# Kernel tuning notes

Measured on AMD Instinct MI355X. Metric: run time of the kernel, lower is better.

## Reference

```python
import jax, jax.numpy as jnp
import numpy as np

D_MODEL = 1024
N_HEADS = 16
RANK = 128
N_COMPRESS = 16
N_KNOWLEDGE = 32768
KNOWLEDGE_K = 8
B, S = 4, 1024
EPS = 1e-5


def setup_inputs() -> dict:
    key = jax.random.key(0)
    ks = jax.random.split(key, 16)
    inp = {
        'x': jax.random.normal(ks[0], (B, S, D_MODEL), jnp.float32),
        'mask': jnp.tril(jnp.ones((S, S), bool))[None, None],  # causal [1,1,S,S]
        'compress_neurons': jax.random.normal(ks[1], (N_COMPRESS, D_MODEL, RANK), jnp.float32) / np.sqrt(D_MODEL),
        'knowledge_K': jax.random.normal(ks[2], (N_KNOWLEDGE, RANK), jnp.float32) * 0.02,
        'knowledge_V': jax.random.normal(ks[3], (N_KNOWLEDGE, D_MODEL), jnp.float32) * 0.02,
        'router_Q': jax.random.normal(ks[4], (D_MODEL, N_COMPRESS), jnp.float32) * 0.02,
        'router_K': jax.random.normal(ks[5], (D_MODEL, N_COMPRESS), jnp.float32) * 0.02,
        'router_V': jax.random.normal(ks[6], (D_MODEL, N_COMPRESS), jnp.float32) * 0.02,
        'router_M': jax.random.normal(ks[7], (D_MODEL, N_COMPRESS), jnp.float32) * 0.02,
        'W_Q': jax.random.normal(ks[8], (RANK, D_MODEL), jnp.float32) / np.sqrt(RANK),
        'W_K': jax.random.normal(ks[9], (RANK, D_MODEL), jnp.float32) / np.sqrt(RANK),
        'W_V': jax.random.normal(ks[10], (RANK, D_MODEL), jnp.float32) / np.sqrt(RANK),
        'W_O': jax.random.normal(ks[11], (D_MODEL, D_MODEL), jnp.float32) / np.sqrt(D_MODEL),
        'ln1_g': jnp.ones((D_MODEL,), jnp.float32),
        'ln1_b': jnp.zeros((D_MODEL,), jnp.float32),
        'ln2_g': jnp.ones((D_MODEL,), jnp.float32),
        'ln2_b': jnp.zeros((D_MODEL,), jnp.float32),
    }
    return inp


def _layernorm(x, g, b):
    mu = x.mean(-1, keepdims=True)
    var = ((x - mu) ** 2).mean(-1, keepdims=True)
    return (x - mu) * jax.lax.rsqrt(var + EPS) * g + b


def _compress(x, router_W, neurons):
    # x: [B,S,D]; router_W: [D,N]; neurons: [N,D,R]
    weights = jax.nn.softmax(x @ router_W, axis=-1)               # [B,S,N]
    all_proj = jnp.einsum('bsd,ndr->bsnr', x, neurons)            # [B,S,N,R]
    return jnp.einsum('bsnr,bsn->bsr', all_proj, weights)         # [B,S,R]


def reference(x, mask, compress_neurons, knowledge_K, knowledge_V,
              router_Q, router_K, router_V, router_M,
              W_Q, W_K, W_V, W_O, ln1_g, ln1_b, ln2_g, ln2_b):
    d_head = D_MODEL // N_HEADS
    h = _layernorm(x, ln1_g, ln1_b)
    # soft-routed low-rank compression for Q/K/V
    hQ = _compress(h, router_Q, compress_neurons)
    hK = _compress(h, router_K, compress_neurons)
    hV = _compress(h, router_V, compress_neurons)
    Q = (hQ @ W_Q).reshape(B, S, N_HEADS, d_head).transpose(0, 2, 1, 3)
    K = (hK @ W_K).reshape(B, S, N_HEADS, d_head).transpose(0, 2, 1, 3)
    V = (hV @ W_V).reshape(B, S, N_HEADS, d_head).transpose(0, 2, 1, 3)
    scores = jnp.einsum('bhqd,bhkd->bhqk', Q, K) / np.sqrt(d_head)
    scores = jnp.where(mask, scores, -jnp.inf)
    attn = jax.nn.softmax(scores, axis=-1)
    attn_out = jnp.einsum('bhqk,bhkd->bhqd', attn, V)
    attn_out = attn_out.transpose(0, 2, 1, 3).reshape(B, S, D_MODEL)
    x = x + attn_out @ W_O
    # knowledge memory
    h2 = _layernorm(x, ln2_g, ln2_b)
    Qm = _compress(h2, router_M, compress_neurons)                # [B,S,R]
    kscores = Qm @ knowledge_K.T / np.sqrt(RANK)                  # [B,S,NK]
    topk_scores, topk_idx = jax.lax.top_k(kscores, KNOWLEDGE_K)
    kweights = jax.nn.softmax(topk_scores, axis=-1)               # [B,S,k]
    selected_V = knowledge_V[topk_idx]                            # [B,S,k,D]
    mem_out = jnp.einsum('bskd,bsk->bsd', selected_V, kweights)
    return x + mem_out
```

## Files before the change

### kernel.cpp

```cpp
#include <hip/hip_runtime.h>
#include <math.h>

#define DM     1024
#define RANK   128
#define NCMP   16
#define NKNOW  32768
#define TOPK   8
#define NROWS  4096
#define NEG_BIG -3.0e38f
#define TK_SPLIT 32
#define TK_KEYS (NKNOW / TK_SPLIT)

typedef __attribute__((ext_vector_type(8))) short s8v;
typedef __attribute__((ext_vector_type(4))) float f4v;

__device__ __forceinline__ unsigned short f2bf(float f) {
  union { float fl; unsigned u; } v; v.fl = f;
  return (unsigned short)((v.u + 0x7FFFu + ((v.u >> 16) & 1u)) >> 16);
}
__device__ __forceinline__ f4v mfma16(s8v a, s8v b, f4v c) {
  return __builtin_amdgcn_mfma_f32_16x16x32_bf16(a, b, c, 0, 0, 0);
}
__device__ __forceinline__ unsigned umed3(unsigned a, unsigned b, unsigned c) {
  unsigned d;
  asm("v_med3_u32 %0, %1, %2, %3" : "=v"(d) : "v"(a), "v"(b), "v"(c));
  return d;
}

__global__ __launch_bounds__(256) void ln_kernel(const float* __restrict__ x,
                                                 const float* __restrict__ g,
                                                 const float* __restrict__ b,
                                                 float* __restrict__ o,
                                                 unsigned short* __restrict__ obf) {
  __shared__ float red1[4], red2[4];
  const int row = blockIdx.x, t = threadIdx.x;
  const float4 v = reinterpret_cast<const float4*>(x + (size_t)row * DM)[t];
  float s = v.x + v.y + v.z + v.w;
#pragma unroll
  for (int m = 1; m <= 32; m <<= 1) s += __shfl_xor(s, m);
  if ((t & 63) == 0) red1[t >> 6] = s;
  __syncthreads();
  const float mu = (red1[0] + red1[1] + red1[2] + red1[3]) * (1.0f / DM);
  const float dx = v.x - mu, dy = v.y - mu, dz = v.z - mu, dw = v.w - mu;
  float ss = dx * dx + dy * dy + dz * dz + dw * dw;
#pragma unroll
  for (int m = 1; m <= 32; m <<= 1) ss += __shfl_xor(ss, m);
  if ((t & 63) == 0) red2[t >> 6] = ss;
  __syncthreads();
  const float var = (red2[0] + red2[1] + red2[2] + red2[3]) * (1.0f / DM);
  const float inv = rsqrtf(var + 1e-5f);
  const float4 g4 = reinterpret_cast<const float4*>(g)[t];
  const float4 b4 = reinterpret_cast<const float4*>(b)[t];
  float4 r;
  r.x = dx * inv * g4.x + b4.x;
  r.y = dy * inv * g4.y + b4.y;
  r.z = dz * inv * g4.z + b4.z;
  r.w = dw * inv * g4.w + b4.w;
  reinterpret_cast<float4*>(o + (size_t)row * DM)[t] = r;
  ushort4 u = make_ushort4(f2bf(r.x), f2bf(r.y), f2bf(r.z), f2bf(r.w));
  reinterpret_cast<ushort4*>(obf + (size_t)row * DM)[t] = u;
}

__global__ __launch_bounds__(256) void tcvt_kernel(const float* __restrict__ in,
                                                   unsigned short* __restrict__ out,
                                                   int K, int N) {
  __shared__ float ld[32][33];
  const int bb = blockIdx.z;
  const int k0 = blockIdx.y * 32, n0 = blockIdx.x * 32;
  const int t = threadIdx.x;
  const float* ib = in + (size_t)bb * K * N;
  unsigned short* ob = out + (size_t)bb * K * N;
  const int kl = t >> 3, nl = (t & 7) * 4;
  const float4 v = *reinterpret_cast<const float4*>(&ib[(size_t)(k0 + kl) * N + n0 + nl]);
  ld[kl][nl] = v.x; ld[kl][nl + 1] = v.y; ld[kl][nl + 2] = v.z; ld[kl][nl + 3] = v.w;
  __syncthreads();
  const int nw = t >> 3, kw = (t & 7) * 4;
  ushort4 o = make_ushort4(f2bf(ld[kw][nw]), f2bf(ld[kw + 1][nw]),
                           f2bf(ld[kw + 2][nw]), f2bf(ld[kw + 3][nw]));
  *reinterpret_cast<ushort4*>(&ob[(size_t)(n0 + nw) * K + k0 + kw]) = o;
}

__global__ __launch_bounds__(256) void vtr_kernel(const unsigned short* __restrict__ V,
                                                  unsigned short* __restrict__ Vt) {
  __shared__ unsigned short ld[32][40];
  const int bh = blockIdx.z, b = bh >> 4, hh = bh & 15;
  const int s0 = blockIdx.x * 32, d0 = blockIdx.y * 32;
  const int t = threadIdx.x;
  const int r = t >> 3, c = (t & 7) * 4;
  *reinterpret_cast<ushort4*>(&ld[r][c]) =
      *reinterpret_cast<const ushort4*>(&V[(size_t)(b * 1024 + s0 + r) * DM + hh * 64 + d0 + c]);
  __syncthreads();
  ushort4 o;
  o.x = ld[c + 0][r]; o.y = ld[c + 1][r]; o.z = ld[c + 2][r]; o.w = ld[c + 3][r];
  *reinterpret_cast<ushort4*>(&Vt[((size_t)bh * 64 + d0 + r) * 1024 + s0 + c]) = o;
}

__global__ __launch_bounds__(256) void cvt_kernel(const float* __restrict__ in,
                                                  unsigned short* __restrict__ out, int n8) {
  const int i = blockIdx.x * 256 + threadIdx.x;
  if (i < n8) {
    const float4 a = reinterpret_cast<const float4*>(in)[2 * i];
    const float4 b = reinterpret_cast<const float4*>(in)[2 * i + 1];
    reinterpret_cast<ushort4*>(out)[2 * i] =
        make_ushort4(f2bf(a.x), f2bf(a.y), f2bf(a.z), f2bf(a.w));
    reinterpret_cast<ushort4*>(out)[2 * i + 1] =
        make_ushort4(f2bf(b.x), f2bf(b.y), f2bf(b.z), f2bf(b.w));
  }
}

__global__ __launch_bounds__(256) void router3_kernel(const float* __restrict__ h,
                                                      const float* __restrict__ R0,
                                                      const float* __restrict__ R1,
                                                      const float* __restrict__ R2,
                                                      float* __restrict__ w0,
                                                      float* __restrict__ w1,
                                                      float* __restrict__ w2) {
  __shared__ float hs[DM];
  __shared__ float red[3][16][17];
  const int row = blockIdx.x, t = threadIdx.x;
  reinterpret_cast<float4*>(hs)[t] = reinterpret_cast<const float4*>(h + (size_t)row * DM)[t];
  __syncthreads();
  const int o = t & 15, seg = t >> 4;
  float a0 = 0.f, a1 = 0.f, a2 = 0.f;
  for (int d = seg * 64; d < seg * 64 + 64; ++d) {
    const float hv = hs[d];
    a0 += hv * R0[d * NCMP + o];
    a1 += hv * R1[d * NCMP + o];
    a2 += hv * R2[d * NCMP + o];
  }
  red[0][seg][o] = a0; red[1][seg][o] = a1; red[2][seg][o] = a2;
  __syncthreads();
  if (t < 48) {
    const int g = t >> 4, oo = t & 15;
    float dot = 0.f;
#pragma unroll
    for (int s = 0; s < 16; ++s) dot += red[g][s][oo];
    float m = dot;
#pragma unroll
    for (int msk = 1; msk < 16; msk <<= 1) m = fmaxf(m, __shfl_xor(m, msk));
    const float e = __expf(dot - m);
    float ssum = e;
#pragma unroll
    for (int msk = 1; msk < 16; msk <<= 1) ssum += __shfl_xor(ssum, msk);
    float* wp = (g == 0) ? w0 : (g == 1) ? w1 : w2;
    wp[(size_t)row * NCMP + oo] = e / ssum;
  }
}

__global__ __launch_bounds__(256) void router_kernel(const float* __restrict__ h,
                                                     const float* __restrict__ R,
                                                     float* __restrict__ w) {
  __shared__ float hs[DM];
  __shared__ float red[16][17];
  const int row = blockIdx.x, t = threadIdx.x;
  reinterpret_cast<float4*>(hs)[t] = reinterpret_cast<const float4*>(h + (size_t)row * DM)[t];
  __syncthreads();
  const int o = t & 15, seg = t >> 4;
  float acc = 0.f;
  for (int d = seg * 64; d < seg * 64 + 64; ++d) acc += hs[d] * R[d * NCMP + o];
  red[seg][o] = acc;
  __syncthreads();
  if (t < 16) {
    float dot = 0.f;
#pragma unroll
    for (int s = 0; s < 16; ++s) dot += red[s][t];
    float m = dot;
#pragma unroll
    for (int msk = 1; msk < 16; msk <<= 1) m = fmaxf(m, __shfl_xor(m, msk));
    const float e = __expf(dot - m);
    float ssum = e;
#pragma unroll
    for (int msk = 1; msk < 16; msk <<= 1) ssum += __shfl_xor(ssum, msk);
    w[(size_t)row * NCMP + t] = e / ssum;
  }
}

template <bool OUT_BF16, bool RES>
__global__ __launch_bounds__(256) void mfma_nt(const unsigned short* __restrict__ A,
                                               const unsigned short* __restrict__ B,
                                               float* __restrict__ Cf,
                                               unsigned short* __restrict__ Cb,
                                               const float* __restrict__ res,
                                               int M, int N, int K, int bshift) {
  __shared__ unsigned short As[128 * 72];
  __shared__ unsigned short Bs[128 * 72];
  const int t = threadIdx.x;
  const int lane = t & 63, w = t >> 6;
  const int wm = w >> 1, wn = w & 1;
  const int bm = blockIdx.y, bn = blockIdx.x;
  const int l15 = lane & 15, l4 = lane >> 4;
  f4v acc[4][4] = {};
  const int sr = t >> 1, sh = t & 1;
  const unsigned short* ga = A + (size_t)(bm * 128 + sr) * K + sh * 32;
  const unsigned short* gb = B + (size_t)(bm >> bshift) * ((size_t)N * K) +
                             (size_t)(bn * 128 + sr) * K + sh * 32;
  for (int k0 = 0; k0 < K; k0 += 64) {
#pragma unroll
    for (int j = 0; j < 4; ++j) {
      *reinterpret_cast<s8v*>(&As[sr * 72 + sh * 32 + j * 8]) =
          *reinterpret_cast<const s8v*>(&ga[k0 + j * 8]);
      *reinterpret_cast<s8v*>(&Bs[sr * 72 + sh * 32 + j * 8]) =
          *reinterpret_cast<const s8v*>(&gb[k0 + j * 8]);
    }
    __syncthreads();
#pragma unroll
    for (int ks = 0; ks < 2; ++ks) {
      s8v af[4], bf[4];
#pragma unroll
      for (int i = 0; i < 4; ++i) {
        af[i] = *reinterpret_cast<const s8v*>(&As[(wm * 64 + i * 16 + l15) * 72 + ks * 32 + l4 * 8]);
        bf[i] = *reinterpret_cast<const s8v*>(&Bs[(wn * 64 + i * 16 + l15) * 72 + ks * 32 + l4 * 8]);
      }
#pragma unroll
      for (int i = 0; i < 4; ++i)
#pragma unroll
        for (int j = 0; j < 4; ++j) acc[i][j] = mfma16(af[i], bf[j], acc[i][j]);
    }
    __syncthreads();
  }
#pragma unroll
  for (int i = 0; i < 4; ++i) {
#pragma unroll
    for (int j = 0; j < 4; ++j) {
#pragma unroll
      for (int r = 0; r < 4; ++r) {
        const int row = bm * 128 + wm * 64 + i * 16 + l4 * 4 + r;
        const int col = bn * 128 + wn * 64 + j * 16 + l15;
        float v = acc[i][j][r];
        if constexpr (RES) v += res[(size_t)row * N + col];
        if constexpr (OUT_BF16) Cb[(size_t)row * N + col] = f2bf(v);
        else Cf[(size_t)row * N + col] = v;
      }
    }
  }
}

__global__ __launch_bounds__(128) void wsum_kernel(const float* __restrict__ ap,
                                                   const float* __restrict__ w0,
                                                   const float* __restrict__ w1,
                                                   const float* __restrict__ w2,
                                                   unsigned short* __restrict__ o0,
                                                   unsigned short* __restrict__ o1,
                                                   unsigned short* __restrict__ o2,
                                                   float scale) {
  const int row = blockIdx.x, r = threadIdx.x;
  float wa[16], wb[16], wc[16];
#pragma unroll
  for (int n = 0; n < 16; ++n) wa[n] = w0[(size_t)row * NCMP + n];
  if (w1) {
#pragma unroll
    for (int n = 0; n < 16; ++n) wb[n] = w1[(size_t)row * NCMP + n];
  }
  if (w2) {
#pragma unroll
    for (int n = 0; n < 16; ++n) wc[n] = w2[(size_t)row * NCMP + n];
  }
  float a0 = 0.f, a1 = 0.f, a2 = 0.f;
  const float* apr = ap + (size_t)row * (NCMP * RANK) + r;
#pragma unroll
  for (int n = 0; n < 16; ++n) {
    const float v = apr[n * RANK];
    a0 += v * wa[n];
    if (w1) a1 += v * wb[n];
    if (w2) a2 += v * wc[n];
  }
  o0[(size_t)row * RANK + r] = f2bf(a0 * scale);
  if (o1) o1[(size_t)row * RANK + r] = f2bf(a1 * scale);
  if (o2) o2[(size_t)row * RANK + r] = f2bf(a2 * scale);
}

__global__ __launch_bounds__(256) void flash_kernel(const unsigned short* __restrict__ Q,
                                                    const unsigned short* __restrict__ K,
                                                    const unsigned short* __restrict__ Vt,
                                                    unsigned short* __restrict__ O) {
  __shared__ unsigned short Qs[64 * 72], Ks[64 * 72], Vs[64 * 72], Ps[64 * 72];
  const int bh = blockIdx.x, qt = blockIdx.y;
  const int b = bh >> 4, hh = bh & 15;
  const int base = b * 1024, q0 = qt * 64, col = hh * 64;
  const int t = threadIdx.x;
  const int lane = t & 63, w = t >> 6;
  const int l15 = lane & 15, l4 = lane >> 4;
  const int sr = t >> 2, soff = (t & 3) * 16;
  const unsigned short* Vh = Vt + (size_t)bh * 64 * 1024;
  *reinterpret_cast<s8v*>(&Qs[sr * 72 + soff]) =
      *reinterpret_cast<const s8v*>(&Q[(size_t)(base + q0 + sr) * DM + col + soff]);
  *reinterpret_cast<s8v*>(&Qs[sr * 72 + soff + 8]) =
      *reinterpret_cast<const s8v*>(&Q[(size_t)(base + q0 + sr) * DM + col + soff + 8]);
  *reinterpret_cast<s8v*>(&Ks[sr * 72 + soff]) =
      *reinterpret_cast<const s8v*>(&K[(size_t)(base + sr) * DM + col + soff]);
  *reinterpret_cast<s8v*>(&Ks[sr * 72 + soff + 8]) =
      *reinterpret_cast<const s8v*>(&K[(size_t)(base + sr) * DM + col + soff + 8]);
  *reinterpret_cast<s8v*>(&Vs[sr * 72 + soff]) =
      *reinterpret_cast<const s8v*>(&Vh[(size_t)sr * 1024 + soff]);
  *reinterpret_cast<s8v*>(&Vs[sr * 72 + soff + 8]) =
      *reinterpret_cast<const s8v*>(&Vh[(size_t)sr * 1024 + soff + 8]);
  float m_r[4], l_r[4];
  f4v o[4] = {};
#pragma unroll
  for (int r = 0; r < 4; ++r) { m_r[r] = NEG_BIG; l_r[r] = 0.f; }
  __syncthreads();
  for (int kt = 0; kt <= qt; ++kt) {
    const int k0 = kt * 64;
    const bool pre = kt < qt;
    s8v stk0, stk1, stv0, stv1;
    if (pre) {
      const int kn = k0 + 64;
      stk0 = *reinterpret_cast<const s8v*>(&K[(size_t)(base + kn + sr) * DM + col + soff]);
      stk1 = *reinterpret_cast<const s8v*>(&K[(size_t)(base + kn + sr) * DM + col + soff + 8]);
      stv0 = *reinterpret_cast<const s8v*>(&Vh[(size_t)sr * 1024 + kn + soff]);
      stv1 = *reinterpret_cast<const s8v*>(&Vh[(size_t)sr * 1024 + kn + soff + 8]);
    }
    f4v s[4] = {};
#pragma unroll
    for (int ks = 0; ks < 2; ++ks) {
      s8v a = *reinterpret_cast<const s8v*>(&Qs[(w * 16 + l15) * 72 + ks * 32 + l4 * 8]);
#pragma unroll
      for (int nj = 0; nj < 4; ++nj) {
        s8v bb = *reinterpret_cast<const s8v*>(&Ks[(nj * 16 + l15) * 72 + ks * 32 + l4 * 8]);
        s[nj] = mfma16(a, bb, s[nj]);
      }
    }
#pragma unroll
    for (int r = 0; r < 4; ++r) {
      const int grow = q0 + w * 16 + l4 * 4 + r;
      float sv[4];
#pragma unroll
      for (int nj = 0; nj < 4; ++nj) {
        const float xx = s[nj][r] * 0.125f;
        const int gcol = k0 + nj * 16 + l15;
        sv[nj] = (gcol <= grow) ? xx : NEG_BIG;
      }
      float mt = fmaxf(fmaxf(sv[0], sv[1]), fmaxf(sv[2], sv[3]));
#pragma unroll
      for (int msk = 1; msk < 16; msk <<= 1) mt = fmaxf(mt, __shfl_xor(mt, msk));
      const float mn = fmaxf(m_r[r], mt);
      const float sc = __expf(m_r[r] - mn);
      m_r[r] = mn;
      float rs = 0.f, pv[4];
#pragma unroll
      for (int nj = 0; nj < 4; ++nj) { pv[nj] = __expf(sv[nj] - mn); rs += pv[nj]; }
#pragma unroll
      for (int msk = 1; msk < 16; msk <<= 1) rs += __shfl_xor(rs, msk);
      l_r[r] = l_r[r] * sc + rs;
#pragma unroll
      for (int nd = 0; nd < 4; ++nd) o[nd][r] *= sc;
#pragma unroll
      for (int nj = 0; nj < 4; ++nj)
        Ps[(w * 16 + l4 * 4 + r) * 72 + nj * 16 + l15] = f2bf(pv[nj]);
    }
#pragma unroll
    for (int ks = 0; ks < 2; ++ks) {
      s8v pa = *reinterpret_cast<const s8v*>(&Ps[(w * 16 + l15) * 72 + ks * 32 + l4 * 8]);
#pragma unroll
      for (int nd = 0; nd < 4; ++nd) {
        s8v vb = *reinterpret_cast<const s8v*>(&Vs[(nd * 16 + l15) * 72 + ks * 32 + l4 * 8]);
        o[nd] = mfma16(pa, vb, o[nd]);
      }
    }
    __syncthreads();
    if (pre) {
      *reinterpret_cast<s8v*>(&Ks[sr * 72 + soff]) = stk0;
      *reinterpret_cast<s8v*>(&Ks[sr * 72 + soff + 8]) = stk1;
      *reinterpret_cast<s8v*>(&Vs[sr * 72 + soff]) = stv0;
      *reinterpret_cast<s8v*>(&Vs[sr * 72 + soff + 8]) = stv1;
    }
    __syncthreads();
  }
#pragma unroll
  for (int nd = 0; nd < 4; ++nd)
#pragma unroll
    for (int r = 0; r < 4; ++r) {
      const int grow = base + q0 + w * 16 + l4 * 4 + r;
      O[(size_t)grow * DM + col + nd * 16 + l15] = f2bf(o[nd][r] / l_r[r]);
    }
}

__global__ __launch_bounds__(256) void topk_kernel(const unsigned short* __restrict__ Qm,
                                                   const unsigned short* __restrict__ kK,
                                                   float* __restrict__ tks,
                                                   int* __restrict__ tki) {
  __shared__ __align__(16) char arena[32768];
  unsigned short* const Kt0 = (unsigned short*)arena;
  unsigned short* const Kt1 = (unsigned short*)(arena + 16384);
  const int rb = blockIdx.x, sp = blockIdx.y;
  const int r0 = rb * 64, kb0 = sp * TK_KEYS;
  const int t = threadIdx.x;
  const int lane = t & 63, w = t >> 6;
  const int l15 = lane & 15, l4 = lane >> 4;
  s8v qf[4];
#pragma unroll
  for (int ks = 0; ks < 4; ++ks)
    qf[ks] = *reinterpret_cast<const s8v*>(
        &Qm[(size_t)(r0 + w * 16 + l15) * RANK + ks * 32 + l4 * 8]);
  unsigned bs0 = 0u, bs1 = 0u, bs2 = 0u, bs3 = 0u, bs4 = 0u, bs5 = 0u, bs6 = 0u, bs7 = 0u;
  const int sk = t >> 2, sslot = t & 3;
  const unsigned short* gk = kK + (size_t)(kb0 + sk) * RANK + sslot * 32;
  const int fbase = ((sk >> 4) * 4 + sslot) * 512 + (sk & 15) * 8;
  const int NCH = TK_KEYS / 64;
  s8v st[4];
#pragma unroll
  for (int j = 0; j < 4; ++j) st[j] = *reinterpret_cast<const s8v*>(&gk[j * 8]);
#pragma unroll
  for (int j = 0; j < 4; ++j)
    *reinterpret_cast<s8v*>(&Kt0[fbase + j * 128]) = st[j];
  __syncthreads();
  for (int ch = 0; ch < NCH; ++ch) {
    const unsigned short* const bufc = (ch & 1) ? Kt1 : Kt0;
    unsigned short* const bufn = (ch & 1) ? Kt0 : Kt1;
    const bool havenext = (ch + 1) < NCH;
    if (havenext) {
      const unsigned short* g = gk + (size_t)(ch + 1) * 64 * RANK;
#pragma unroll
      for (int j = 0; j < 4; ++j) st[j] = *reinterpret_cast<const s8v*>(&g[j * 8]);
    }
    f4v acc[4] = {};
#pragma unroll
    for (int kt = 0; kt < 4; ++kt) {
#pragma unroll
      for (int ks = 0; ks < 4; ++ks) {
        s8v a = *reinterpret_cast<const s8v*>(&bufc[(kt * 4 + ks) * 512 + lane * 8]);
        acc[kt] = mfma16(a, qf[ks], acc[kt]);
      }
    }
    const unsigned invbase = 2047u - (unsigned)(ch * 64 + l4 * 4);
#pragma unroll
    for (int kt = 0; kt < 4; ++kt) {
#pragma unroll
      for (int r = 0; r < 4; ++r) {
        const unsigned u = __float_as_uint(acc[kt][r]);
        const unsigned ord = u ^ ((unsigned)((int)u >> 31) | 0x80000000u);
        const unsigned pk = (ord & 0xFFFFF800u) | (invbase - (unsigned)(kt * 16 + r));
        bs7 = umed3(bs6, pk, bs7);
        bs6 = umed3(bs5, pk, bs6);
        bs5 = umed3(bs4, pk, bs5);
        bs4 = umed3(bs3, pk, bs4);
        bs3 = umed3(bs2, pk, bs3);
        bs2 = umed3(bs1, pk, bs2);
        bs1 = umed3(bs0, pk, bs1);
        bs0 = max(bs0, pk);
      }
    }
    if (havenext) {
#pragma unroll
      for (int j = 0; j < 4; ++j)
        *reinterpret_cast<s8v*>(&bufn[fbase + j * 128]) = st[j];
    }
    __syncthreads();
  }
  unsigned* const M = (unsigned*)arena;
  const int row = w * 16 + l15;
  {
    unsigned* mp = M + row * 33 + l4 * 8;
    mp[0] = bs0; mp[1] = bs1; mp[2] = bs2; mp[3] = bs3;
    mp[4] = bs4; mp[5] = bs5; mp[6] = bs6; mp[7] = bs7;
  }
  __syncthreads();
  if (t < 64) {
    const unsigned* mr = M + t * 33;
    int h0 = 0, h1 = 0, h2 = 0, h3 = 0;
    const size_t oo = ((size_t)sp * NROWS + r0 + t) * TOPK;
    for (int k = 0; k < TOPK; ++k) {
      const unsigned c0 = (h0 < 8) ? mr[0 + h0] : 0u;
      const unsigned c1 = (h1 < 8) ? mr[8 + h1] : 0u;
      const unsigned c2 = (h2 < 8) ? mr[16 + h2] : 0u;
      const unsigned c3 = (h3 < 8) ? mr[24 + h3] : 0u;
      const unsigned m01 = (c0 >= c1) ? c0 : c1; const int l01 = (c0 >= c1) ? 0 : 1;
      const unsigned m23 = (c2 >= c3) ? c2 : c3; const int l23 = (c2 >= c3) ? 2 : 3;
      const unsigned bst = (m01 >= m23) ? m01 : m23;
      const int bl = (m01 >= m23) ? l01 : l23;
      const unsigned hi = bst & 0xFFFFF800u;
      const unsigned vb = (hi & 0x80000000u) ? (hi & 0x7FFFFFFFu) : ~hi;
      tks[oo + k] = __uint_as_float(vb);
      tki[oo + k] = kb0 + (int)((~bst) & 0x7FFu);
      h0 += (bl == 0); h1 += (bl == 1); h2 += (bl == 2); h3 += (bl == 3);
    }
  }
}

__global__ __launch_bounds__(256) void gather_kernel(const float* __restrict__ tks,
                                                     const int* __restrict__ tki,
                                                     const float* __restrict__ kV,
                                                     float* __restrict__ out) {
  __shared__ float ls[TK_SPLIT * TOPK];
  __shared__ int li[TK_SPLIT * TOPK];
  __shared__ float selv[TOPK];
  __shared__ int seli[TOPK];
  __shared__ float wsel[TOPK];
  const int row = blockIdx.x, t = threadIdx.x;
  if (t < TK_SPLIT * TOPK) {
    const int l = t >> 3, k = t & 7;
    ls[t] = tks[((size_t)l * NROWS + row) * TOPK + k];
    li[t] = tki[((size_t)l * NROWS + row) * TOPK + k];
  }
  __syncthreads();
  if (t < TK_SPLIT * TOPK) {
    const float v = ls[t];
    const int myid = li[t];
    int rank = 0;
    for (int j = 0; j < TK_SPLIT * TOPK; ++j) {
      const float u = ls[j];
      rank += (u > v) || (u == v && li[j] < myid);
    }
    if (rank < TOPK) { selv[rank] = v; seli[rank] = myid; }
  }
  __syncthreads();
  if (t == 0) {
    const float m = selv[0];
    float sum = 0.f, e[TOPK];
#pragma unroll
    for (int k = 0; k < TOPK; ++k) { e[k] = __expf(selv[k] - m); sum += e[k]; }
    const float inv = 1.f / sum;
#pragma unroll
    for (int k = 0; k < TOPK; ++k) wsel[k] = e[k] * inv;
  }
  __syncthreads();
  float4 accv = reinterpret_cast<float4*>(out + (size_t)row * DM)[t];
#pragma unroll
  for (int k = 0; k < TOPK; ++k) {
    const float4 v4 = reinterpret_cast<const float4*>(kV + (size_t)seli[k] * DM)[t];
    const float wk = wsel[k];
    accv.x += wk * v4.x; accv.y += wk * v4.y; accv.z += wk * v4.z; accv.w += wk * v4.w;
  }
  reinterpret_cast<float4*>(out + (size_t)row * DM)[t] = accv;
}

extern "C" void kernel_launch(void* const* d_in, const int* in_sizes, int n_in,
                              void* d_out, int out_size, void* d_ws, size_t ws_size,
                              hipStream_t stream) {
  (void)in_sizes; (void)n_in; (void)out_size; (void)ws_size;
  const float* x    = (const float*)d_in[0];
  const float* neur = (const float*)d_in[2];
  const float* kK   = (const float*)d_in[3];
  const float* kV   = (const float*)d_in[4];
  const float* rQ   = (const float*)d_in[5];
  const float* rK   = (const float*)d_in[6];
  const float* rV   = (const float*)d_in[7];
  const float* rM   = (const float*)d_in[8];
  const float* WQ   = (const float*)d_in[9];
  const float* WK   = (const float*)d_in[10];
  const float* WV   = (const float*)d_in[11];
  const float* WO   = (const float*)d_in[12];
  const float* g1   = (const float*)d_in[13];
  const float* b1   = (const float*)d_in[14];
  const float* g2   = (const float*)d_in[15];
  const float* b2   = (const float*)d_in[16];
  float* out = (float*)d_out;

  char* base = (char*)d_ws;
  auto alloc = [&](size_t bytes) { char* r = base; base += (bytes + 255) & ~(size_t)255; return r; };
  float*          h     = (float*)alloc((size_t)NROWS * DM * 4);
  unsigned short* hbf   = (unsigned short*)alloc((size_t)NROWS * DM * 2);
  float*          ap    = (float*)alloc((size_t)NROWS * NCMP * RANK * 4);
  unsigned short* neurT = (unsigned short*)alloc((size_t)NCMP * RANK * DM * 2);
  unsigned short* WQKVt = (unsigned short*)alloc((size_t)3 * DM * RANK * 2);
  unsigned short* WOt   = (unsigned short*)alloc((size_t)DM * DM * 2);
  unsigned short* kKb   = (unsigned short*)alloc((size_t)NKNOW * RANK * 2);
  unsigned short* hQKVb = (unsigned short*)alloc((size_t)3 * NROWS * RANK * 2);
  unsigned short* Qmb   = (unsigned short*)alloc((size_t)NROWS * RANK * 2);
  unsigned short* Vtb   = (unsigned short*)alloc((size_t)NROWS * DM * 2);
  float* wQw = (float*)alloc((size_t)NROWS * NCMP * 4);
  float* wKw = (float*)alloc((size_t)NROWS * NCMP * 4);
  float* wVw = (float*)alloc((size_t)NROWS * NCMP * 4);
  float* wMw = (float*)alloc((size_t)NROWS * NCMP * 4);
  float* tks = (float*)alloc((size_t)TK_SPLIT * NROWS * TOPK * 4);
  int*   tki = (int*)alloc((size_t)TK_SPLIT * NROWS * TOPK * 4);
  unsigned short* Qb = (unsigned short*)ap;
  unsigned short* Kb = Qb + (size_t)NROWS * DM;
  unsigned short* Vb = Kb + (size_t)NROWS * DM;
  unsigned short* attnb = hbf;
  unsigned short* hQb = hQKVb;
  unsigned short* hKb = hQKVb + (size_t)NROWS * RANK;
  unsigned short* hVb = hQKVb + (size_t)2 * NROWS * RANK;

  cvt_kernel<<<(NKNOW * RANK / 8 + 255) / 256, 256, 0, stream>>>(kK, kKb, NKNOW * RANK / 8);
  tcvt_kernel<<<dim3(RANK / 32, DM / 32, NCMP), 256, 0, stream>>>(neur, neurT, DM, RANK);
  tcvt_kernel<<<dim3(DM / 32, RANK / 32, 1), 256, 0, stream>>>(WQ, WQKVt, RANK, DM);
  tcvt_kernel<<<dim3(DM / 32, RANK / 32, 1), 256, 0, stream>>>(WK, WQKVt + (size_t)DM * RANK, RANK, DM);
  tcvt_kernel<<<dim3(DM / 32, RANK / 32, 1), 256, 0, stream>>>(WV, WQKVt + (size_t)2 * DM * RANK, RANK, DM);
  tcvt_kernel<<<dim3(DM / 32, DM / 32, 1), 256, 0, stream>>>(WO, WOt, DM, DM);

  ln_kernel<<<NROWS, 256, 0, stream>>>(x, g1, b1, h, hbf);
  mfma_nt<false, false><<<dim3(16, 32), 256, 0, stream>>>(hbf, neurT, ap, nullptr, nullptr,
                                                          NROWS, NCMP * RANK, DM, 30);
  router3_kernel<<<NROWS, 256, 0, stream>>>(h, rQ, rK, rV, wQw, wKw, wVw);
  wsum_kernel<<<NROWS, 128, 0, stream>>>(ap, wQw, wKw, wVw, hQb, hKb, hVb, 1.0f);
  mfma_nt<true, false><<<dim3(8, 96), 256, 0, stream>>>(hQKVb, WQKVt, nullptr, Qb, nullptr,
                                                        3 * NROWS, DM, RANK, 5);
  vtr_kernel<<<dim3(32, 2, 64), 256, 0, stream>>>(Vb, Vtb);
  flash_kernel<<<dim3(64, 16), 256, 0, stream>>>(Qb, Kb, Vtb, attnb);
  mfma_nt<false, true><<<dim3(8, 32), 256, 0, stream>>>(attnb, WOt, out, nullptr, x,
                                                        NROWS, DM, DM, 30);

  ln_kernel<<<NROWS, 256, 0, stream>>>(out, g2, b2, h, hbf);
  mfma_nt<false, false><<<dim3(16, 32), 256, 0, stream>>>(hbf, neurT, ap, nullptr, nullptr,
                                                          NROWS, NCMP * RANK, DM, 30);
  router_kernel<<<NROWS, 256, 0, stream>>>(h, rM, wMw);
  wsum_kernel<<<NROWS, 128, 0, stream>>>(ap, wMw, nullptr, nullptr, Qmb, nullptr, nullptr,
                                         0.08838834764831845f );
  topk_kernel<<<dim3(64, TK_SPLIT), 256, 0, stream>>>(Qmb, kKb, tks, tki);
  gather_kernel<<<NROWS, 256, 0, stream>>>(tks, tki, kV, out);
}
```

Before: 354.6 us.

## Use direct global-to-LDS loads with swizzle and store intermediates in bf16

Replaces register-staged global-to-shared copies in the GEMM and top-k kernels with global_load_lds 16-byte transfers into an XOR-swizzled, unpadded shared layout, so loads no longer pass through VGPRs and avoid bank conflicts. It also stops writing the fp32 layernorm output and stores the compress projection (all_proj) in bf16 instead of fp32, with the routers and weighted sum reading bf16. This halves or removes several large intermediate write and read streams, at the cost of lower precision in the router inputs and the projection.

```diff
diff --git a/kernel.cpp b/kernel.cpp
--- a/kernel.cpp
+++ b/kernel.cpp
@@ -18,6 +18,9 @@
   union { float fl; unsigned u; } v; v.fl = f;
   return (unsigned short)((v.u + 0x7FFFu + ((v.u >> 16) & 1u)) >> 16);
 }
+__device__ __forceinline__ float bf2f(unsigned short u) {
+  return __uint_as_float((unsigned)u << 16);
+}
 __device__ __forceinline__ f4v mfma16(s8v a, s8v b, f4v c) {
   return __builtin_amdgcn_mfma_f32_16x16x32_bf16(a, b, c, 0, 0, 0);
 }
@@ -26,11 +29,15 @@
   asm("v_med3_u32 %0, %1, %2, %3" : "=v"(d) : "v"(a), "v"(b), "v"(c));
   return d;
 }
+__device__ __forceinline__ void gload16(const unsigned short* g, unsigned short* l) {
+  __builtin_amdgcn_global_load_lds(
+      (const __attribute__((address_space(1))) unsigned int*)(g),
+      (__attribute__((address_space(3))) unsigned int*)(l), 16, 0, 0);
+}
 
 __global__ __launch_bounds__(256) void ln_kernel(const float* __restrict__ x,
                                                  const float* __restrict__ g,
                                                  const float* __restrict__ b,
-                                                 float* __restrict__ o,
                                                  unsigned short* __restrict__ obf) {
   __shared__ float red1[4], red2[4];
   const int row = blockIdx.x, t = threadIdx.x;
@@ -51,13 +58,8 @@
   const float inv = rsqrtf(var + 1e-5f);
   const float4 g4 = reinterpret_cast<const float4*>(g)[t];
   const float4 b4 = reinterpret_cast<const float4*>(b)[t];
-  float4 r;
-  r.x = dx * inv * g4.x + b4.x;
-  r.y = dy * inv * g4.y + b4.y;
-  r.z = dz * inv * g4.z + b4.z;
-  r.w = dw * inv * g4.w + b4.w;
-  reinterpret_cast<float4*>(o + (size_t)row * DM)[t] = r;
-  ushort4 u = make_ushort4(f2bf(r.x), f2bf(r.y), f2bf(r.z), f2bf(r.w));
+  ushort4 u = make_ushort4(f2bf(dx * inv * g4.x + b4.x), f2bf(dy * inv * g4.y + b4.y),
+                           f2bf(dz * inv * g4.z + b4.z), f2bf(dw * inv * g4.w + b4.w));
   reinterpret_cast<ushort4*>(obf + (size_t)row * DM)[t] = u;
 }
 
@@ -108,7 +110,7 @@
   }
 }
 
-__global__ __launch_bounds__(256) void router3_kernel(const float* __restrict__ h,
+__global__ __launch_bounds__(256) void router3_kernel(const unsigned short* __restrict__ h,
                                                       const float* __restrict__ R0,
                                                       const float* __restrict__ R1,
                                                       const float* __restrict__ R2,
@@ -118,7 +120,11 @@
   __shared__ float hs[DM];
   __shared__ float red[3][16][17];
   const int row = blockIdx.x, t = threadIdx.x;
-  reinterpret_cast<float4*>(hs)[t] = reinterpret_cast<const float4*>(h + (size_t)row * DM)[t];
+  {
+    const ushort4 u = reinterpret_cast<const ushort4*>(h + (size_t)row * DM)[t];
+    hs[t * 4 + 0] = bf2f(u.x); hs[t * 4 + 1] = bf2f(u.y);
+    hs[t * 4 + 2] = bf2f(u.z); hs[t * 4 + 3] = bf2f(u.w);
+  }
   __syncthreads();
   const int o = t & 15, seg = t >> 4;
   float a0 = 0.f, a1 = 0.f, a2 = 0.f;
@@ -147,13 +153,17 @@
   }
 }
 
-__global__ __launch_bounds__(256) void router_kernel(const float* __restrict__ h,
+__global__ __launch_bounds__(256) void router_kernel(const unsigned short* __restrict__ h,
                                                      const float* __restrict__ R,
                                                      float* __restrict__ w) {
   __shared__ float hs[DM];
   __shared__ float red[16][17];
   const int row = blockIdx.x, t = threadIdx.x;
-  reinterpret_cast<float4*>(hs)[t] = reinterpret_cast<const float4*>(h + (size_t)row * DM)[t];
+  {
+    const ushort4 u = reinterpret_cast<const ushort4*>(h + (size_t)row * DM)[t];
+    hs[t * 4 + 0] = bf2f(u.x); hs[t * 4 + 1] = bf2f(u.y);
+    hs[t * 4 + 2] = bf2f(u.z); hs[t * 4 + 3] = bf2f(u.w);
+  }
   __syncthreads();
   const int o = t & 15, seg = t >> 4;
   float acc = 0.f;
@@ -182,34 +192,36 @@
                                                unsigned short* __restrict__ Cb,
                                                const float* __restrict__ res,
                                                int M, int N, int K, int bshift) {
-  __shared__ unsigned short As[128 * 72];
-  __shared__ unsigned short Bs[128 * 72];
+  __shared__ unsigned short As[128 * 64];
+  __shared__ unsigned short Bs[128 * 64];
   const int t = threadIdx.x;
   const int lane = t & 63, w = t >> 6;
   const int wm = w >> 1, wn = w & 1;
   const int bm = blockIdx.y, bn = blockIdx.x;
   const int l15 = lane & 15, l4 = lane >> 4;
   f4v acc[4][4] = {};
-  const int sr = t >> 1, sh = t & 1;
-  const unsigned short* ga = A + (size_t)(bm * 128 + sr) * K + sh * 32;
+  const int srow = w * 32 + (lane >> 3);
+  const int scol = ((lane & 7) ^ (lane >> 3)) * 8;
+  const unsigned short* ga = A + (size_t)(bm * 128 + srow) * K + scol;
   const unsigned short* gb = B + (size_t)(bm >> bshift) * ((size_t)N * K) +
-                             (size_t)(bn * 128 + sr) * K + sh * 32;
+                             (size_t)(bn * 128 + srow) * K + scol;
+  unsigned short* const lA = &As[w * 2048];
+  unsigned short* const lB = &Bs[w * 2048];
   for (int k0 = 0; k0 < K; k0 += 64) {
 #pragma unroll
     for (int j = 0; j < 4; ++j) {
-      *reinterpret_cast<s8v*>(&As[sr * 72 + sh * 32 + j * 8]) =
-          *reinterpret_cast<const s8v*>(&ga[k0 + j * 8]);
-      *reinterpret_cast<s8v*>(&Bs[sr * 72 + sh * 32 + j * 8]) =
-          *reinterpret_cast<const s8v*>(&gb[k0 + j * 8]);
+      gload16(ga + (size_t)j * 8 * K + k0, lA + j * 512);
+      gload16(gb + (size_t)j * 8 * K + k0, lB + j * 512);
     }
     __syncthreads();
 #pragma unroll
     for (int ks = 0; ks < 2; ++ks) {
       s8v af[4], bf[4];
+      const int sc = (ks * 32 + l4 * 8) ^ ((l15 & 7) * 8);
 #pragma unroll
       for (int i = 0; i < 4; ++i) {
-        af[i] = *reinterpret_cast<const s8v*>(&As[(wm * 64 + i * 16 + l15) * 72 + ks * 32 + l4 * 8]);
-        bf[i] = *reinterpret_cast<const s8v*>(&Bs[(wn * 64 + i * 16 + l15) * 72 + ks * 32 + l4 * 8]);
+        af[i] = *reinterpret_cast<const s8v*>(&As[(wm * 64 + i * 16 + l15) * 64 + sc]);
+        bf[i] = *reinterpret_cast<const s8v*>(&Bs[(wn * 64 + i * 16 + l15) * 64 + sc]);
       }
 #pragma unroll
       for (int i = 0; i < 4; ++i)
@@ -235,7 +247,7 @@
   }
 }
 
-__global__ __launch_bounds__(128) void wsum_kernel(const float* __restrict__ ap,
+__global__ __launch_bounds__(128) void wsum_kernel(const unsigned short* __restrict__ ap,
                                                    const float* __restrict__ w0,
                                                    const float* __restrict__ w1,
                                                    const float* __restrict__ w2,
@@ -256,10 +268,10 @@
     for (int n = 0; n < 16; ++n) wc[n] = w2[(size_t)row * NCMP + n];
   }
   float a0 = 0.f, a1 = 0.f, a2 = 0.f;
-  const float* apr = ap + (size_t)row * (NCMP * RANK) + r;
+  const unsigned short* apr = ap + (size_t)row * (NCMP * RANK) + r;
 #pragma unroll
   for (int n = 0; n < 16; ++n) {
-    const float v = apr[n * RANK];
+    const float v = bf2f(apr[n * RANK]);
     a0 += v * wa[n];
     if (w1) a1 += v * wb[n];
     if (w2) a2 += v * wc[n];
@@ -393,25 +405,20 @@
     qf[ks] = *reinterpret_cast<const s8v*>(
         &Qm[(size_t)(r0 + w * 16 + l15) * RANK + ks * 32 + l4 * 8]);
   unsigned bs0 = 0u, bs1 = 0u, bs2 = 0u, bs3 = 0u, bs4 = 0u, bs5 = 0u, bs6 = 0u, bs7 = 0u;
-  const int sk = t >> 2, sslot = t & 3;
-  const unsigned short* gk = kK + (size_t)(kb0 + sk) * RANK + sslot * 32;
-  const int fbase = ((sk >> 4) * 4 + sslot) * 512 + (sk & 15) * 8;
+  const unsigned short* gkl = kK + (size_t)(kb0 + w * 16 + l15) * RANK + l4 * 8;
+  unsigned short* const lw0 = Kt0 + w * 2048;
+  unsigned short* const lw1 = Kt1 + w * 2048;
   const int NCH = TK_KEYS / 64;
-  s8v st[4];
-#pragma unroll
-  for (int j = 0; j < 4; ++j) st[j] = *reinterpret_cast<const s8v*>(&gk[j * 8]);
-#pragma unroll
-  for (int j = 0; j < 4; ++j)
-    *reinterpret_cast<s8v*>(&Kt0[fbase + j * 128]) = st[j];
+#pragma unroll
+  for (int j = 0; j < 4; ++j) gload16(gkl + j * 32, lw0 + j * 512);
   __syncthreads();
   for (int ch = 0; ch < NCH; ++ch) {
     const unsigned short* const bufc = (ch & 1) ? Kt1 : Kt0;
-    unsigned short* const bufn = (ch & 1) ? Kt0 : Kt1;
-    const bool havenext = (ch + 1) < NCH;
-    if (havenext) {
-      const unsigned short* g = gk + (size_t)(ch + 1) * 64 * RANK;
-#pragma unroll
-      for (int j = 0; j < 4; ++j) st[j] = *reinterpret_cast<const s8v*>(&g[j * 8]);
+    unsigned short* const lwn = (ch & 1) ? lw0 : lw1;
+    if (ch + 1 < NCH) {
+      const unsigned short* g = gkl + (size_t)(ch + 1) * 64 * RANK;
+#pragma unroll
+      for (int j = 0; j < 4; ++j) gload16(g + j * 32, lwn + j * 512);
     }
     f4v acc[4] = {};
 #pragma unroll
@@ -439,11 +446,6 @@
         bs1 = umed3(bs0, pk, bs1);
         bs0 = max(bs0, pk);
       }
-    }
-    if (havenext) {
-#pragma unroll
-      for (int j = 0; j < 4; ++j)
-        *reinterpret_cast<s8v*>(&bufn[fbase + j * 128]) = st[j];
     }
     __syncthreads();
   }
@@ -548,9 +550,8 @@
 
   char* base = (char*)d_ws;
   auto alloc = [&](size_t bytes) { char* r = base; base += (bytes + 255) & ~(size_t)255; return r; };
-  float*          h     = (float*)alloc((size_t)NROWS * DM * 4);
   unsigned short* hbf   = (unsigned short*)alloc((size_t)NROWS * DM * 2);
-  float*          ap    = (float*)alloc((size_t)NROWS * NCMP * RANK * 4);
+  unsigned short* apb   = (unsigned short*)alloc((size_t)3 * NROWS * DM * 2);
   unsigned short* neurT = (unsigned short*)alloc((size_t)NCMP * RANK * DM * 2);
   unsigned short* WQKVt = (unsigned short*)alloc((size_t)3 * DM * RANK * 2);
   unsigned short* WOt   = (unsigned short*)alloc((size_t)DM * DM * 2);
@@ -564,7 +565,7 @@
   float* wMw = (float*)alloc((size_t)NROWS * NCMP * 4);
   float* tks = (float*)alloc((size_t)TK_SPLIT * NROWS * TOPK * 4);
   int*   tki = (int*)alloc((size_t)TK_SPLIT * NROWS * TOPK * 4);
-  unsigned short* Qb = (unsigned short*)ap;
+  unsigned short* Qb = apb;
   unsigned short* Kb = Qb + (size_t)NROWS * DM;
   unsigned short* Vb = Kb + (size_t)NROWS * DM;
   unsigned short* attnb = hbf;
@@ -579,11 +580,11 @@
   tcvt_kernel<<<dim3(DM / 32, RANK / 32, 1), 256, 0, stream>>>(WV, WQKVt + (size_t)2 * DM * RANK, RANK, DM);
   tcvt_kernel<<<dim3(DM / 32, DM / 32, 1), 256, 0, stream>>>(WO, WOt, DM, DM);
 
-  ln_kernel<<<NROWS, 256, 0, stream>>>(x, g1, b1, h, hbf);
-  mfma_nt<false, false><<<dim3(16, 32), 256, 0, stream>>>(hbf, neurT, ap, nullptr, nullptr,
-                                                          NROWS, NCMP * RANK, DM, 30);
-  router3_kernel<<<NROWS, 256, 0, stream>>>(h, rQ, rK, rV, wQw, wKw, wVw);
-  wsum_kernel<<<NROWS, 128, 0, stream>>>(ap, wQw, wKw, wVw, hQb, hKb, hVb, 1.0f);
+  ln_kernel<<<NROWS, 256, 0, stream>>>(x, g1, b1, hbf);
+  mfma_nt<true, false><<<dim3(16, 32), 256, 0, stream>>>(hbf, neurT, nullptr, apb, nullptr,
+                                                         NROWS, NCMP * RANK, DM, 30);
+  router3_kernel<<<NROWS, 256, 0, stream>>>(hbf, rQ, rK, rV, wQw, wKw, wVw);
+  wsum_kernel<<<NROWS, 128, 0, stream>>>(apb, wQw, wKw, wVw, hQb, hKb, hVb, 1.0f);
   mfma_nt<true, false><<<dim3(8, 96), 256, 0, stream>>>(hQKVb, WQKVt, nullptr, Qb, nullptr,
                                                         3 * NROWS, DM, RANK, 5);
   vtr_kernel<<<dim3(32, 2, 64), 256, 0, stream>>>(Vb, Vtb);
@@ -591,11 +592,11 @@
   mfma_nt<false, true><<<dim3(8, 32), 256, 0, stream>>>(attnb, WOt, out, nullptr, x,
                                                         NROWS, DM, DM, 30);
 
-  ln_kernel<<<NROWS, 256, 0, stream>>>(out, g2, b2, h, hbf);
-  mfma_nt<false, false><<<dim3(16, 32), 256, 0, stream>>>(hbf, neurT, ap, nullptr, nullptr,
-                                                          NROWS, NCMP * RANK, DM, 30);
-  router_kernel<<<NROWS, 256, 0, stream>>>(h, rM, wMw);
-  wsum_kernel<<<NROWS, 128, 0, stream>>>(ap, wMw, nullptr, nullptr, Qmb, nullptr, nullptr,
+  ln_kernel<<<NROWS, 256, 0, stream>>>(out, g2, b2, hbf);
+  mfma_nt<true, false><<<dim3(16, 32), 256, 0, stream>>>(hbf, neurT, nullptr, apb, nullptr,
+                                                         NROWS, NCMP * RANK, DM, 30);
+  router_kernel<<<NROWS, 256, 0, stream>>>(hbf, rM, wMw);
+  wsum_kernel<<<NROWS, 128, 0, stream>>>(apb, wMw, nullptr, nullptr, Qmb, nullptr, nullptr,
                                          0.08838834764831845f );
   topk_kernel<<<dim3(64, TK_SPLIT), 256, 0, stream>>>(Qmb, kKb, tks, tki);
   gather_kernel<<<NROWS, 256, 0, stream>>>(tks, tki, kV, out);
```

Measured after the change: 342.7 us. -3.4%, faster.
